# Kernel tuning notes

Hardware: AMD Instinct MI355X
Metric: run time of the kernel (lower is better)

The kernel has to match this reference:

```python
import jax, jax.numpy as jnp
import numpy as np

B, L, H = 16, 2048, 1024

def setup_inputs() -> dict:
    key = jax.random.key(0)
    ks = jax.random.split(key, 8)
    s = 1.0 / np.sqrt(H)
    return {
        "query": jax.random.normal(ks[0], (B, L, H), jnp.float32),
        "key_t": jax.random.normal(ks[1], (B, L, H), jnp.float32),
        "value": jax.random.normal(ks[2], (B, L, H), jnp.float32),
        # nn.Linear(H, H, bias=False) weights, stored torch-style [out, in]
        "Wq": jax.random.uniform(ks[3], (H, H), jnp.float32, -s, s),
        "Wk": jax.random.uniform(ks[4], (H, H), jnp.float32, -s, s),
        "bias": jax.random.uniform(ks[5], (H,), jnp.float32, -0.1, 0.1),
        # nn.Linear(H, 1): weight [1, H] -> stored as vector [H], plus scalar bias
        "w_score": jax.random.uniform(ks[6], (H,), jnp.float32, -s, s),
        "b_score": jax.random.uniform(ks[7], (1,), jnp.float32, -s, s),
    }

def reference(query, key_t, value, Wq, Wk, bias, w_score, b_score):
    # score = score_proj(tanh(key_proj(key) + query_proj(query) + bias)).squeeze(-1)
    h = jnp.tanh(jnp.einsum('blh,oh->blo', key_t, Wk)
                 + jnp.einsum('blh,oh->blo', query, Wq)
                 + bias)                                  # [B, L, H]
    score = jnp.einsum('blh,h->bl', h, w_score) + b_score  # [B, L]
    attn = jax.nn.softmax(score, axis=-1)                  # [B, L]
    # bmm(attn[:,None,:], value) -> [B,1,H]; sum over dim=1 (size 1) is identity
    context = jnp.einsum('bl,blh->bh', attn, value)[:, None, :]  # [B, 1, H]
    return context, attn
```

## Files before the change

kernel.cpp:

```cpp
#include <hip/hip_runtime.h>
#include <hip/hip_bf16.h>
#include <math.h>

#define B_SZ 16
#define L_SZ 2048
#define H_SZ 1024
#define M_TOT (B_SZ * L_SZ)
#define N_TOT H_SZ
#define KD (2 * H_SZ)
#define LC 16
#define LCHUNK (L_SZ / LC)

#define BM2 256
#define BN2 256
#define BK2 64
#define NT2 (KD / BK2)
#define NBN2 (N_TOT / BN2)
#define NBM2 (M_TOT / BM2)

typedef short short8 __attribute__((ext_vector_type(8)));
typedef float f32x4 __attribute__((ext_vector_type(4)));

#define GL16(gp, lp)                                                        \
    __builtin_amdgcn_global_load_lds(                                       \
        (const __attribute__((address_space(1))) unsigned int*)(gp),        \
        (__attribute__((address_space(3))) unsigned int*)(lp), 16, 0, 0)

#define BARRIER() __builtin_amdgcn_s_barrier()
#define SCHEDB()  __builtin_amdgcn_sched_barrier(0)
#define LGKM0()   asm volatile("s_waitcnt lgkmcnt(0)" ::: "memory")
#define VMCNT4()  asm volatile("s_waitcnt vmcnt(4)" ::: "memory")
#define VMCNT12() asm volatile("s_waitcnt vmcnt(12)" ::: "memory")
#define VMCNT0()  asm volatile("s_waitcnt vmcnt(0)" ::: "memory")

static __device__ __forceinline__ short8 pack8(float4 x, float4 y) {
    unsigned w0, w1, w2, w3;
    asm("v_cvt_pk_bf16_f32 %0, %1, %2" : "=v"(w0) : "v"(x.x), "v"(x.y));
    asm("v_cvt_pk_bf16_f32 %0, %1, %2" : "=v"(w1) : "v"(x.z), "v"(x.w));
    asm("v_cvt_pk_bf16_f32 %0, %1, %2" : "=v"(w2) : "v"(y.x), "v"(y.y));
    asm("v_cvt_pk_bf16_f32 %0, %1, %2" : "=v"(w3) : "v"(y.z), "v"(y.w));
    int4 q{(int)w0, (int)w1, (int)w2, (int)w3};
    return __builtin_bit_cast(short8, q);
}

static __device__ __forceinline__ float fast_tanh(float x) {
    float e = __expf(2.0f * x);
    return 1.0f - 2.0f * __builtin_amdgcn_rcpf(e + 1.0f);
}

__global__ __launch_bounds__(256) void conv_w(
    const float* __restrict__ Wq, const float* __restrict__ Wk,
    unsigned short* __restrict__ Wb)
{
    int idx = blockIdx.x * 256 + threadIdx.x;
    int e0 = idx * 8;
    int o  = e0 >> 11;
    int kk = e0 & 2047;
    const float* src = (kk < H_SZ) ? (Wk + (size_t)o * H_SZ + kk)
                                   : (Wq + (size_t)o * H_SZ + (kk - H_SZ));
    float4 x = ((const float4*)src)[0];
    float4 y = ((const float4*)src)[1];
    *(short8*)(Wb + e0) = pack8(x, y);
}

__global__ __launch_bounds__(512, 2) void score_gemm_8ph(
    const float* __restrict__ keyg,
    const float* __restrict__ qryg,
    const unsigned short* __restrict__ Wb,
    const float* __restrict__ bias,
    const float* __restrict__ wscore,
    float* __restrict__ spart)
{
    extern __shared__ char smem[];
    char* Albase = smem;
    char* Blbase = smem + 65536;

    const int t    = threadIdx.x;
    const int lane = t & 63;
    const int wid  = t >> 6;
    const int wr   = wid >> 2;
    const int wc   = wid & 3;

    const int id  = blockIdx.x;
    const int xcd = id & 7;
    const int j   = id >> 3;
    const int bn  = j & 3;
    const int bm  = xcd * 16 + (j >> 2);
    const int r0  = bm * BM2;
    const int c0  = bn * BN2;

    const int srow = lane >> 2;
    const int scol = ((lane & 3) * 8) ^ ((lane >= 32) ? 16 : 0);
    const size_t gB0 = (size_t)(c0 + (wid)     * 16 + srow) * KD + scol;
    const size_t gB1 = (size_t)(c0 + (8 + wid) * 16 + srow) * KD + scol;

    const int fr  = lane & 15;
    const int fk8 = (lane >> 4) * 8;
    const int subbyte = (fr * 64 + fk8 * 2) ^ ((fr & 8) << 2);
    const char* aL = Albase + wr * 8192 + subbyte;
    const char* bL = Blbase + wc * 4096 + subbyte;

    const int arow0 = r0 + wid * 16 + (lane >> 2);
    const int arow1 = r0 + (8 + wid) * 16 + (lane >> 2);
    const int acsub = (lane & 3) * 8;
    const int awbyte = (lane * 16) ^ (lane & 32);

#define ALOAD(rr, khalf, kt_) do {                                           \
    int koff = (((kt_) & 31) * 64) + (khalf) * 32 + acsub;                   \
    const float* base_ = (koff < H_SZ) ? (keyg + koff)                       \
                                       : (qryg + (koff - H_SZ));             \
    const float* p0_ = base_ + (size_t)arow0 * H_SZ;                         \
    const float* p1_ = base_ + (size_t)arow1 * H_SZ;                         \
    rr[0] = ((const float4*)p0_)[0]; rr[1] = ((const float4*)p0_)[1];        \
    rr[2] = ((const float4*)p1_)[0]; rr[3] = ((const float4*)p1_)[1];        \
} while (0)
#define AWRITE(rr, buf, khalf) do {                                          \
    char* d_ = Albase + (((buf)*2 + (khalf))*16 + wid)*1024 + awbyte;        \
    *(short8*)d_            = pack8(rr[0], rr[1]);                           \
    *(short8*)(d_ + 8*1024) = pack8(rr[2], rr[3]);                           \
} while (0)
#define STAGE_B(buf, khalf, kt_) do {                                        \
    int kpos = (((kt_) & 31) * 64) + (khalf) * 32;                           \
    GL16(Wb + gB0 + kpos, Blbase + (((buf)*2 + (khalf))*16 + wid)*1024);     \
    GL16(Wb + gB1 + kpos, Blbase + (((buf)*2 + (khalf))*16 + 8 + wid)*1024); \
} while (0)

    float4 rA0[4], rA1[4];
    short8 a_f[4], b_f0[4], b_f1[4];
    f32x4 acc[8][4] = {};

#define LDA4(buf, ks, mh) do { _Pragma("unroll")                             \
    for (int m = 0; m < 4; ++m)                                              \
        a_f[m] = *(const short8*)(aL +                                       \
            (((buf)*2 + (ks))*16 + (mh)*4 + m) * 1024); } while (0)
#define LDB4(dst, buf, ks) do { _Pragma("unroll")                            \
    for (int n = 0; n < 4; ++n)                                              \
        dst[n] = *(const short8*)(bL +                                       \
            (((buf)*2 + (ks))*16 + n) * 1024); } while (0)
#define MM16(bff, mh) do {                                                   \
    __builtin_amdgcn_s_setprio(1);                                           \
    _Pragma("unroll")                                                        \
    for (int m = 0; m < 4; ++m) { _Pragma("unroll")                          \
        for (int n = 0; n < 4; ++n)                                          \
            acc[(mh)*4 + m][n] = __builtin_amdgcn_mfma_f32_16x16x32_bf16(    \
                a_f[m], bff[n], acc[(mh)*4 + m][n], 0, 0, 0); }              \
    __builtin_amdgcn_s_setprio(0); } while (0)

#define TILE(buf, u) do {                                                    \
    LDA4(buf, 0, 0); LDB4(b_f0, buf, 0); ALOAD(rA0, 0, (u)+2);               \
    BARRIER(); LGKM0(); MM16(b_f0, 0);                                       \
    SCHEDB(); AWRITE(rA1, 1-(buf), 1); BARRIER();                            \
    LDA4(buf, 0, 1); STAGE_B(1-(buf), 1, (u)+1);                             \
    BARRIER(); LGKM0(); MM16(b_f0, 1); VMCNT12(); BARRIER();                 \
    LDA4(buf, 1, 0); LDB4(b_f1, buf, 1); ALOAD(rA1, 1, (u)+2);               \
    BARRIER(); LGKM0(); MM16(b_f1, 0);                                       \
    SCHEDB(); AWRITE(rA0, buf, 0); BARRIER();                                \
    LDA4(buf, 1, 1); STAGE_B(buf, 0, (u)+2);                                 \
    BARRIER(); LGKM0(); MM16(b_f1, 1); VMCNT12(); BARRIER();                 \
} while (0)

    STAGE_B(0, 0, 0); STAGE_B(0, 1, 0); STAGE_B(1, 0, 1);
    ALOAD(rA0, 0, 0); ALOAD(rA1, 1, 0);
    AWRITE(rA0, 0, 0); AWRITE(rA1, 0, 1);
    ALOAD(rA0, 0, 1);  AWRITE(rA0, 1, 0);
    ALOAD(rA1, 1, 1);
    VMCNT4();
    LGKM0();
    BARRIER();

    for (int it = 0; it < NT2; it += 2) {
        TILE(0, it);
        TILE(1, it + 1);
    }

    VMCNT0();
    __syncthreads();

    float* part = (float*)smem;
    const int fg = lane >> 4;
    float wsv[4], bsv[4];
    #pragma unroll
    for (int n = 0; n < 4; ++n) {
        int cg = c0 + wc * 64 + n * 16 + fr;
        wsv[n] = wscore[cg];
        bsv[n] = bias[cg];
    }
    #pragma unroll
    for (int mm = 0; mm < 8; ++mm) {
        #pragma unroll
        for (int r = 0; r < 4; ++r) {
            float s = 0.f;
            #pragma unroll
            for (int n = 0; n < 4; ++n)
                s += wsv[n] * fast_tanh(acc[mm][n][r] + bsv[n]);
            s += __shfl_xor(s, 1, 64);
            s += __shfl_xor(s, 2, 64);
            s += __shfl_xor(s, 4, 64);
            s += __shfl_xor(s, 8, 64);
            if (fr == 0)
                part[wc * 256 + wr * 128 + mm * 16 + fg * 4 + r] = s;
        }
    }
    __syncthreads();
    if (t < 256) {
        float v = part[t] + part[256 + t] + part[512 + t] + part[768 + t];
        spart[(size_t)(r0 + t) * 4 + bn] = v;
    }

#undef ALOAD
#undef AWRITE
#undef STAGE_B
#undef LDA4
#undef LDB4
#undef MM16
#undef TILE
}

__global__ __launch_bounds__(256) void softmax_k(
    const float* __restrict__ spart,
    float* __restrict__ attn)
{
    __shared__ float sc[L_SZ];
    __shared__ float red[8];
    const int b = blockIdx.x, t = threadIdx.x;
    const int lane = t & 63, wid = t >> 6;

    float lmax = -1e30f;
    #pragma unroll
    for (int i = 0; i < 8; ++i) {
        int l = t + i * 256;
        float4 u = *(const float4*)(spart + ((size_t)b * L_SZ + l) * 4);
        float s = (u.x + u.y) + (u.z + u.w);
        sc[l] = s;
        lmax = fmaxf(lmax, s);
    }
    #pragma unroll
    for (int off = 32; off; off >>= 1) lmax = fmaxf(lmax, __shfl_xor(lmax, off, 64));
    if (lane == 0) red[wid] = lmax;
    __syncthreads();
    float bmax = fmaxf(fmaxf(red[0], red[1]), fmaxf(red[2], red[3]));

    float lsum = 0.f;
    #pragma unroll
    for (int i = 0; i < 8; ++i) {
        int l = t + i * 256;
        float e = expf(sc[l] - bmax);
        sc[l] = e;
        lsum += e;
    }
    #pragma unroll
    for (int off = 32; off; off >>= 1) lsum += __shfl_xor(lsum, off, 64);
    if (lane == 0) red[4 + wid] = lsum;
    __syncthreads();
    float inv = 1.f / (((red[4] + red[5]) + (red[6] + red[7])));

    #pragma unroll
    for (int i = 0; i < 8; ++i) {
        int l = t + i * 256;
        attn[(size_t)b * L_SZ + l] = sc[l] * inv;
    }
}

__global__ __launch_bounds__(256) void ctx_part_k(
    const float* __restrict__ attn, const float* __restrict__ value,
    float* __restrict__ cpart)
{
    const int bid = blockIdx.x;
    const int b   = bid >> 6;
    const int rem = bid & 63;
    const int hc  = rem >> 4;
    const int lc  = rem & 15;
    const int h   = hc * 256 + threadIdx.x;

    const float* ap = attn + (size_t)b * L_SZ + lc * LCHUNK;
    const float* vp = value + ((size_t)b * L_SZ + lc * LCHUNK) * H_SZ + h;
    float acc = 0.f;
    #pragma unroll 4
    for (int l = 0; l < LCHUNK; ++l)
        acc += ap[l] * vp[(size_t)l * H_SZ];
    cpart[((size_t)(b * LC + lc)) * H_SZ + h] = acc;
}

__global__ __launch_bounds__(256) void ctx_reduce_k(
    const float* __restrict__ cpart, float* __restrict__ ctx)
{
    const int idx = blockIdx.x * 256 + threadIdx.x;
    const int b = idx >> 10, h = idx & 1023;
    float s = 0.f;
    #pragma unroll
    for (int lc = 0; lc < LC; ++lc)
        s += cpart[((size_t)(b * LC + lc)) * H_SZ + h];
    ctx[idx] = s;
}

extern "C" void kernel_launch(void* const* d_in, const int* in_sizes, int n_in,
                              void* d_out, int out_size, void* d_ws, size_t ws_size,
                              hipStream_t stream) {
    const float* query  = (const float*)d_in[0];
    const float* key_t  = (const float*)d_in[1];
    const float* value  = (const float*)d_in[2];
    const float* Wq     = (const float*)d_in[3];
    const float* Wk     = (const float*)d_in[4];
    const float* bias   = (const float*)d_in[5];
    const float* wscore = (const float*)d_in[6];

    float* out      = (float*)d_out;
    float* ctx_out  = out;
    float* attn_out = out + B_SZ * H_SZ;

    char* ws = (char*)d_ws;
    unsigned short* Wb = (unsigned short*)ws;
    float* spart = (float*)(ws + 4ull * 1024 * 1024);
    float* cpart = (float*)(ws + 5ull * 1024 * 1024);

    (void)hipFuncSetAttribute((const void*)score_gemm_8ph,
                              hipFuncAttributeMaxDynamicSharedMemorySize, 131072);

    conv_w<<<1024, 256, 0, stream>>>(Wq, Wk, Wb);

    score_gemm_8ph<<<NBM2 * NBN2, 512, 131072, stream>>>(
        key_t, query, Wb, bias, wscore, spart);

    softmax_k<<<B_SZ, 256, 0, stream>>>(spart, attn_out);
    ctx_part_k<<<B_SZ * 4 * LC, 256, 0, stream>>>(attn_out, value, cpart);
    ctx_reduce_k<<<(B_SZ * H_SZ) / 256, 256, 0, stream>>>(cpart, ctx_out);
}
```

Before: 204.6 us.

## Shrink score GEMM tiles to 128x256x32 with single-stage pipeline for higher occupancy

Replaces the 256x256x64 eight-phase score GEMM with a 128x256 tile, K-step 32 and a simpler double-buffered pipeline using 48KB of LDS. Launch bounds go from 2 to 4 blocks per CU and the grid doubles. The aim is to hide latency through occupancy rather than hand-scheduled phases. In exchange, arithmetic intensity per tile drops, so the B weight tile is reloaded twice as often, and there are more barriers per unit of work.

```diff
diff --git a/kernel.cpp b/kernel.cpp
--- a/kernel.cpp
+++ b/kernel.cpp
@@ -11,12 +11,12 @@
 #define LC 16
 #define LCHUNK (L_SZ / LC)
 
-#define BM2 256
-#define BN2 256
-#define BK2 64
-#define NT2 (KD / BK2)
-#define NBN2 (N_TOT / BN2)
-#define NBM2 (M_TOT / BM2)
+#define BM3 128
+#define BN3 256
+#define BK3 32
+#define NT3 (KD / BK3)
+#define NBN3 (N_TOT / BN3)
+#define NBM3 (M_TOT / BM3)
 
 typedef short short8 __attribute__((ext_vector_type(8)));
 typedef float f32x4 __attribute__((ext_vector_type(4)));
@@ -29,8 +29,7 @@
 #define BARRIER() __builtin_amdgcn_s_barrier()
 #define SCHEDB()  __builtin_amdgcn_sched_barrier(0)
 #define LGKM0()   asm volatile("s_waitcnt lgkmcnt(0)" ::: "memory")
-#define VMCNT4()  asm volatile("s_waitcnt vmcnt(4)" ::: "memory")
-#define VMCNT12() asm volatile("s_waitcnt vmcnt(12)" ::: "memory")
+#define VMCNT2()  asm volatile("s_waitcnt vmcnt(2)" ::: "memory")
 #define VMCNT0()  asm volatile("s_waitcnt vmcnt(0)" ::: "memory")
 
 static __device__ __forceinline__ short8 pack8(float4 x, float4 y) {
@@ -63,7 +62,7 @@
     *(short8*)(Wb + e0) = pack8(x, y);
 }
 
-__global__ __launch_bounds__(512, 2) void score_gemm_8ph(
+__global__ __launch_bounds__(512, 4) void score_gemm_dual(
     const float* __restrict__ keyg,
     const float* __restrict__ qryg,
     const unsigned short* __restrict__ Wb,
@@ -73,7 +72,7 @@
 {
     extern __shared__ char smem[];
     char* Albase = smem;
-    char* Blbase = smem + 65536;
+    char* Blbase = smem + 16384;
 
     const int t    = threadIdx.x;
     const int lane = t & 63;
@@ -85,9 +84,9 @@
     const int xcd = id & 7;
     const int j   = id >> 3;
     const int bn  = j & 3;
-    const int bm  = xcd * 16 + (j >> 2);
-    const int r0  = bm * BM2;
-    const int c0  = bn * BN2;
+    const int bm  = xcd * 32 + (j >> 2);
+    const int r0  = bm * BM3;
+    const int c0  = bn * BN3;
 
     const int srow = lane >> 2;
     const int scol = ((lane & 3) * 8) ^ ((lane >= 32) ? 16 : 0);
@@ -97,80 +96,68 @@
     const int fr  = lane & 15;
     const int fk8 = (lane >> 4) * 8;
     const int subbyte = (fr * 64 + fk8 * 2) ^ ((fr & 8) << 2);
-    const char* aL = Albase + wr * 8192 + subbyte;
+    const char* aL = Albase + wr * 4096 + subbyte;
     const char* bL = Blbase + wc * 4096 + subbyte;
 
-    const int arow0 = r0 + wid * 16 + (lane >> 2);
-    const int arow1 = r0 + (8 + wid) * 16 + (lane >> 2);
+    const int arow  = r0 + (t >> 2);
     const int acsub = (lane & 3) * 8;
     const int awbyte = (lane * 16) ^ (lane & 32);
 
-#define ALOAD(rr, khalf, kt_) do {                                           \
-    int koff = (((kt_) & 31) * 64) + (khalf) * 32 + acsub;                   \
+#define ALOAD(rr, kt_) do {                                                  \
+    int koff = (((kt_) & 63) * 32) + acsub;                                  \
     const float* base_ = (koff < H_SZ) ? (keyg + koff)                       \
                                        : (qryg + (koff - H_SZ));             \
-    const float* p0_ = base_ + (size_t)arow0 * H_SZ;                         \
-    const float* p1_ = base_ + (size_t)arow1 * H_SZ;                         \
-    rr[0] = ((const float4*)p0_)[0]; rr[1] = ((const float4*)p0_)[1];        \
-    rr[2] = ((const float4*)p1_)[0]; rr[3] = ((const float4*)p1_)[1];        \
+    const float* p_ = base_ + (size_t)arow * H_SZ;                           \
+    rr[0] = ((const float4*)p_)[0]; rr[1] = ((const float4*)p_)[1];          \
 } while (0)
-#define AWRITE(rr, buf, khalf) do {                                          \
-    char* d_ = Albase + (((buf)*2 + (khalf))*16 + wid)*1024 + awbyte;        \
-    *(short8*)d_            = pack8(rr[0], rr[1]);                           \
-    *(short8*)(d_ + 8*1024) = pack8(rr[2], rr[3]);                           \
+#define AWRITE(rr, buf) do {                                                 \
+    char* d_ = Albase + (((buf)*8 + wid)*1024) + awbyte;                     \
+    *(short8*)d_ = pack8(rr[0], rr[1]);                                      \
 } while (0)
-#define STAGE_B(buf, khalf, kt_) do {                                        \
-    int kpos = (((kt_) & 31) * 64) + (khalf) * 32;                           \
-    GL16(Wb + gB0 + kpos, Blbase + (((buf)*2 + (khalf))*16 + wid)*1024);     \
-    GL16(Wb + gB1 + kpos, Blbase + (((buf)*2 + (khalf))*16 + 8 + wid)*1024); \
+#define STAGE_B(buf, kt_) do {                                               \
+    int kpos = ((kt_) & 63) * 32;                                            \
+    GL16(Wb + gB0 + kpos, Blbase + (((buf)*16 + wid)*1024));                 \
+    GL16(Wb + gB1 + kpos, Blbase + (((buf)*16 + 8 + wid)*1024));             \
 } while (0)
 
-    float4 rA0[4], rA1[4];
-    short8 a_f[4], b_f0[4], b_f1[4];
-    f32x4 acc[8][4] = {};
-
-#define LDA4(buf, ks, mh) do { _Pragma("unroll")                             \
+    float4 rA0[2], rA1[2];
+    short8 a_f[4], b_f[4];
+    f32x4 acc[4][4] = {};
+
+#define LDA4(buf) do { _Pragma("unroll")                                     \
     for (int m = 0; m < 4; ++m)                                              \
-        a_f[m] = *(const short8*)(aL +                                       \
-            (((buf)*2 + (ks))*16 + (mh)*4 + m) * 1024); } while (0)
-#define LDB4(dst, buf, ks) do { _Pragma("unroll")                            \
+        a_f[m] = *(const short8*)(aL + (((buf)*8 + m) * 1024)); } while (0)
+#define LDB4(buf) do { _Pragma("unroll")                                     \
     for (int n = 0; n < 4; ++n)                                              \
-        dst[n] = *(const short8*)(bL +                                       \
-            (((buf)*2 + (ks))*16 + n) * 1024); } while (0)
-#define MM16(bff, mh) do {                                                   \
+        b_f[n] = *(const short8*)(bL + (((buf)*16 + n) * 1024)); } while (0)
+#define MM16() do {                                                          \
     __builtin_amdgcn_s_setprio(1);                                           \
     _Pragma("unroll")                                                        \
     for (int m = 0; m < 4; ++m) { _Pragma("unroll")                          \
         for (int n = 0; n < 4; ++n)                                          \
-            acc[(mh)*4 + m][n] = __builtin_amdgcn_mfma_f32_16x16x32_bf16(    \
-                a_f[m], bff[n], acc[(mh)*4 + m][n], 0, 0, 0); }              \
+            acc[m][n] = __builtin_amdgcn_mfma_f32_16x16x32_bf16(             \
+                a_f[m], b_f[n], acc[m][n], 0, 0, 0); }                       \
     __builtin_amdgcn_s_setprio(0); } while (0)
 
-#define TILE(buf, u) do {                                                    \
-    LDA4(buf, 0, 0); LDB4(b_f0, buf, 0); ALOAD(rA0, 0, (u)+2);               \
-    BARRIER(); LGKM0(); MM16(b_f0, 0);                                       \
-    SCHEDB(); AWRITE(rA1, 1-(buf), 1); BARRIER();                            \
-    LDA4(buf, 0, 1); STAGE_B(1-(buf), 1, (u)+1);                             \
-    BARRIER(); LGKM0(); MM16(b_f0, 1); VMCNT12(); BARRIER();                 \
-    LDA4(buf, 1, 0); LDB4(b_f1, buf, 1); ALOAD(rA1, 1, (u)+2);               \
-    BARRIER(); LGKM0(); MM16(b_f1, 0);                                       \
-    SCHEDB(); AWRITE(rA0, buf, 0); BARRIER();                                \
-    LDA4(buf, 1, 1); STAGE_B(buf, 0, (u)+2);                                 \
-    BARRIER(); LGKM0(); MM16(b_f1, 1); VMCNT12(); BARRIER();                 \
+#define TILE(buf, u, rNew, rOld) do {                                        \
+    AWRITE(rOld, 1-(buf));                          \
+    LDA4(buf); LDB4(buf);                                                    \
+    STAGE_B(1-(buf), (u)+1);                                                 \
+    ALOAD(rNew, (u)+2);                                                      \
+    BARRIER(); LGKM0(); MM16(); VMCNT2(); BARRIER();                         \
 } while (0)
 
-    STAGE_B(0, 0, 0); STAGE_B(0, 1, 0); STAGE_B(1, 0, 1);
-    ALOAD(rA0, 0, 0); ALOAD(rA1, 1, 0);
-    AWRITE(rA0, 0, 0); AWRITE(rA1, 0, 1);
-    ALOAD(rA0, 0, 1);  AWRITE(rA0, 1, 0);
-    ALOAD(rA1, 1, 1);
-    VMCNT4();
+    STAGE_B(0, 0);
+    ALOAD(rA0, 0);
+    AWRITE(rA0, 0);
+    ALOAD(rA1, 1);
+    VMCNT2();
     LGKM0();
     BARRIER();
 
-    for (int it = 0; it < NT2; it += 2) {
-        TILE(0, it);
-        TILE(1, it + 1);
+    for (int it = 0; it < NT3; it += 2) {
+        TILE(0, it,     rA0, rA1);
+        TILE(1, it + 1, rA1, rA0);
     }
 
     VMCNT0();
@@ -186,24 +173,24 @@
         bsv[n] = bias[cg];
     }
     #pragma unroll
-    for (int mm = 0; mm < 8; ++mm) {
+    for (int m = 0; m < 4; ++m) {
         #pragma unroll
         for (int r = 0; r < 4; ++r) {
             float s = 0.f;
             #pragma unroll
             for (int n = 0; n < 4; ++n)
-                s += wsv[n] * fast_tanh(acc[mm][n][r] + bsv[n]);
+                s += wsv[n] * fast_tanh(acc[m][n][r] + bsv[n]);
             s += __shfl_xor(s, 1, 64);
             s += __shfl_xor(s, 2, 64);
             s += __shfl_xor(s, 4, 64);
             s += __shfl_xor(s, 8, 64);
             if (fr == 0)
-                part[wc * 256 + wr * 128 + mm * 16 + fg * 4 + r] = s;
+                part[wc * 128 + wr * 64 + m * 16 + fg * 4 + r] = s;
         }
     }
     __syncthreads();
-    if (t < 256) {
-        float v = part[t] + part[256 + t] + part[512 + t] + part[768 + t];
+    if (t < BM3) {
+        float v = part[t] + part[128 + t] + part[256 + t] + part[384 + t];
         spart[(size_t)(r0 + t) * 4 + bn] = v;
     }
 
@@ -313,12 +300,12 @@
     float* spart = (float*)(ws + 4ull * 1024 * 1024);
     float* cpart = (float*)(ws + 5ull * 1024 * 1024);
 
-    (void)hipFuncSetAttribute((const void*)score_gemm_8ph,
-                              hipFuncAttributeMaxDynamicSharedMemorySize, 131072);
+    (void)hipFuncSetAttribute((const void*)score_gemm_dual,
+                              hipFuncAttributeMaxDynamicSharedMemorySize, 49152);
 
     conv_w<<<1024, 256, 0, stream>>>(Wq, Wk, Wb);
 
-    score_gemm_8ph<<<NBM2 * NBN2, 512, 131072, stream>>>(
+    score_gemm_dual<<<NBM3 * NBN3, 512, 49152, stream>>>(
         key_t, query, Wb, bias, wscore, spart);
 
     softmax_k<<<B_SZ, 256, 0, stream>>>(spart, attn_out);
```

Result: slower. 223.4 us (+9.2%).

## Restructure GEMM main loop from eight phases per tile pair to four

Applied to the files above, without the earlier changes.

Reorganizes the score GEMM's inner loop so each K-half loads all eight A fragments and four B fragments at once and issues 32 MFMAs in one block, instead of splitting them into 16-MFMA phases. This halves the number of barriers and waitcnt points per tile and changes when the B staging and A global loads are issued relative to compute. It costs more live registers for A fragments and gives a coarser interleave of memory ops with MFMA, which may hurt latency hiding at two waves per SIMD.

```diff
diff --git a/kernel.cpp b/kernel.cpp
--- a/kernel.cpp
+++ b/kernel.cpp
@@ -30,7 +30,7 @@
 #define SCHEDB()  __builtin_amdgcn_sched_barrier(0)
 #define LGKM0()   asm volatile("s_waitcnt lgkmcnt(0)" ::: "memory")
 #define VMCNT4()  asm volatile("s_waitcnt vmcnt(4)" ::: "memory")
-#define VMCNT12() asm volatile("s_waitcnt vmcnt(12)" ::: "memory")
+#define VMCNT10() asm volatile("s_waitcnt vmcnt(10)" ::: "memory")
 #define VMCNT0()  asm volatile("s_waitcnt vmcnt(0)" ::: "memory")
 
 static __device__ __forceinline__ short8 pack8(float4 x, float4 y) {
@@ -63,7 +63,7 @@
     *(short8*)(Wb + e0) = pack8(x, y);
 }
 
-__global__ __launch_bounds__(512, 2) void score_gemm_8ph(
+__global__ __launch_bounds__(512, 2) void score_gemm_4ph(
     const float* __restrict__ keyg,
     const float* __restrict__ qryg,
     const unsigned short* __restrict__ Wb,
@@ -126,37 +126,35 @@
 } while (0)
 
     float4 rA0[4], rA1[4];
-    short8 a_f[4], b_f0[4], b_f1[4];
+    short8 a_f[8], b_f[4];
     f32x4 acc[8][4] = {};
 
-#define LDA4(buf, ks, mh) do { _Pragma("unroll")                             \
-    for (int m = 0; m < 4; ++m)                                              \
+#define LDA8(buf, ks) do { _Pragma("unroll")                                 \
+    for (int m = 0; m < 8; ++m)                                              \
         a_f[m] = *(const short8*)(aL +                                       \
-            (((buf)*2 + (ks))*16 + (mh)*4 + m) * 1024); } while (0)
-#define LDB4(dst, buf, ks) do { _Pragma("unroll")                            \
+            (((buf)*2 + (ks))*16 + m) * 1024); } while (0)
+#define LDB4(buf, ks) do { _Pragma("unroll")                                 \
     for (int n = 0; n < 4; ++n)                                              \
-        dst[n] = *(const short8*)(bL +                                       \
+        b_f[n] = *(const short8*)(bL +                                       \
             (((buf)*2 + (ks))*16 + n) * 1024); } while (0)
-#define MM16(bff, mh) do {                                                   \
+#define MM32() do {                                                          \
     __builtin_amdgcn_s_setprio(1);                                           \
     _Pragma("unroll")                                                        \
-    for (int m = 0; m < 4; ++m) { _Pragma("unroll")                          \
+    for (int mm = 0; mm < 8; ++mm) { _Pragma("unroll")                       \
         for (int n = 0; n < 4; ++n)                                          \
-            acc[(mh)*4 + m][n] = __builtin_amdgcn_mfma_f32_16x16x32_bf16(    \
-                a_f[m], bff[n], acc[(mh)*4 + m][n], 0, 0, 0); }              \
+            acc[mm][n] = __builtin_amdgcn_mfma_f32_16x16x32_bf16(            \
+                a_f[mm], b_f[n], acc[mm][n], 0, 0, 0); }                     \
     __builtin_amdgcn_s_setprio(0); } while (0)
 
 #define TILE(buf, u) do {                                                    \
-    LDA4(buf, 0, 0); LDB4(b_f0, buf, 0); ALOAD(rA0, 0, (u)+2);               \
-    BARRIER(); LGKM0(); MM16(b_f0, 0);                                       \
-    SCHEDB(); AWRITE(rA1, 1-(buf), 1); BARRIER();                            \
-    LDA4(buf, 0, 1); STAGE_B(1-(buf), 1, (u)+1);                             \
-    BARRIER(); LGKM0(); MM16(b_f0, 1); VMCNT12(); BARRIER();                 \
-    LDA4(buf, 1, 0); LDB4(b_f1, buf, 1); ALOAD(rA1, 1, (u)+2);               \
-    BARRIER(); LGKM0(); MM16(b_f1, 0);                                       \
-    SCHEDB(); AWRITE(rA0, buf, 0); BARRIER();                                \
-    LDA4(buf, 1, 1); STAGE_B(buf, 0, (u)+2);                                 \
-    BARRIER(); LGKM0(); MM16(b_f1, 1); VMCNT12(); BARRIER();                 \
+    LDA8(buf, 0); LDB4(buf, 0);                                              \
+    STAGE_B(1-(buf), 1, (u)+1); ALOAD(rA0, 0, (u)+2);                        \
+    BARRIER(); LGKM0(); MM32();                                              \
+    SCHEDB(); AWRITE(rA1, 1-(buf), 1); VMCNT10(); BARRIER();                 \
+    LDA8(buf, 1); LDB4(buf, 1);                                              \
+    STAGE_B(buf, 0, (u)+2); ALOAD(rA1, 1, (u)+2);                            \
+    BARRIER(); LGKM0(); MM32();                                              \
+    SCHEDB(); AWRITE(rA0, buf, 0); VMCNT10(); BARRIER();                     \
 } while (0)
 
     STAGE_B(0, 0, 0); STAGE_B(0, 1, 0); STAGE_B(1, 0, 1);
@@ -210,9 +208,9 @@
 #undef ALOAD
 #undef AWRITE
 #undef STAGE_B
-#undef LDA4
+#undef LDA8
 #undef LDB4
-#undef MM16
+#undef MM32
 #undef TILE
 }
 
@@ -313,12 +311,12 @@
     float* spart = (float*)(ws + 4ull * 1024 * 1024);
     float* cpart = (float*)(ws + 5ull * 1024 * 1024);
 
-    (void)hipFuncSetAttribute((const void*)score_gemm_8ph,
+    (void)hipFuncSetAttribute((const void*)score_gemm_4ph,
                               hipFuncAttributeMaxDynamicSharedMemorySize, 131072);
 
     conv_w<<<1024, 256, 0, stream>>>(Wq, Wk, Wb);
 
-    score_gemm_8ph<<<NBM2 * NBN2, 512, 131072, stream>>>(
+    score_gemm_4ph<<<NBM2 * NBN2, 512, 131072, stream>>>(
         key_t, query, Wb, bias, wscore, spart);
 
     softmax_k<<<B_SZ, 256, 0, stream>>>(spart, attn_out);
```

Result: slower. 210.2 us (+2.7%).
